# Performance work log

Measured on AMD Instinct MI355X. Metric: run time of the kernel, lower is better.

## Reference

```python
import jax, jax.numpy as jnp
import numpy as np


def setup_inputs() -> dict:
    key = jax.random.key(0)
    k1, k2 = jax.random.split(key)
    B, S_ENC, S_DEC, D = 8, 2048, 2048, 512
    enc_outputs = jax.random.normal(k1, (B, S_ENC, D), dtype=jnp.float32)
    dec_outputs = jax.random.normal(k2, (B, S_DEC, D), dtype=jnp.float32)
    return {"enc_outputs": enc_outputs, "dec_outputs": dec_outputs}


def reference(enc_outputs, dec_outputs):
    # scores: [B, S_dec, S_enc] = dec @ enc^T  (no scaling, no mask — matches original)
    s_t = jnp.einsum('bqd,bkd->bqk', dec_outputs, enc_outputs)
    a_t = jax.nn.softmax(s_t, axis=-1)
    # context: [B, S_dec, D]
    c_t = jnp.einsum('bqk,bkd->bqd', a_t, enc_outputs)
    return c_t
```

## Files before the change

kernel.cpp:

```cpp
#include <hip/hip_runtime.h>
#include <cstdint>
#include <cstddef>

#define Bb 8
#define Ss 2048
#define Dd 512

typedef _Float16 half8 __attribute__((ext_vector_type(8)));
typedef _Float16 half4_ __attribute__((ext_vector_type(4)));
typedef _Float16 half2_t __attribute__((ext_vector_type(2)));
typedef float f32x4 __attribute__((ext_vector_type(4)));

static __device__ __forceinline__ void gload_lds16(const void* g, void* l) {
  __builtin_amdgcn_global_load_lds((const __attribute__((address_space(1))) void*)g,
                                   (__attribute__((address_space(3))) void*)l,
                                   16, 0, 0);
}

__global__ void k0_cvt(const float* __restrict__ in, _Float16* __restrict__ out, int n8) {
  int i = blockIdx.x * blockDim.x + threadIdx.x;
  if (i >= n8) return;
  const float4* p = (const float4*)in + (size_t)i * 2;
  float4 a = p[0], b = p[1];
  half8 h;
  h[0] = (_Float16)a.x; h[1] = (_Float16)a.y; h[2] = (_Float16)a.z; h[3] = (_Float16)a.w;
  h[4] = (_Float16)b.x; h[5] = (_Float16)b.y; h[6] = (_Float16)b.z; h[7] = (_Float16)b.w;
  *(half8*)(out + (size_t)i * 8) = h;
}

__global__ void k0_enc(const float* __restrict__ enc, _Float16* __restrict__ enc16,
                       _Float16* __restrict__ encT) {
  __shared__ float tile[32][33];
  int bid = blockIdx.x;
  int b = bid & 7, kt = (bid >> 3) & 63, dt = bid >> 9;
  int key0 = kt * 32, d0 = dt * 32;
  int t = threadIdx.x;
  const float* src = enc + ((size_t)b * Ss + key0) * Dd + d0;
  _Float16* dst = enc16 + ((size_t)b * Ss + key0) * Dd + d0;
#pragma unroll
  for (int p = 0; p < 4; ++p) {
    int idx = t + p * 256;
    int r = idx >> 5, c = idx & 31;
    float v = src[(size_t)r * Dd + c];
    tile[r][c] = v;
    dst[(size_t)r * Dd + c] = (_Float16)v;
  }
  __syncthreads();
  {
    int dr = t >> 3, kq = t & 7;
    _Float16* o = encT + ((size_t)b * Dd + d0 + dr) * Ss + key0 + kq * 4;
    half4_ v;
#pragma unroll
    for (int j = 0; j < 4; ++j) v[j] = (_Float16)tile[kq * 4 + j][dr];
    *(half4_*)o = v;
  }
}

__launch_bounds__(256, 2)
__global__ void k1_qk(const _Float16* __restrict__ A, const _Float16* __restrict__ Bm,
                      _Float16* __restrict__ S, half2_t* __restrict__ pms) {
  __shared__ __align__(16) _Float16 lA[128 * 64];
  __shared__ __align__(16) _Float16 lB[128 * 64];
  int bid = blockIdx.x;
  int b = bid & 7;
  int t = bid >> 3;
  int tm = t & 15, tn = t >> 4;
  int tid = threadIdx.x;
  int w = tid >> 6, L = tid & 63;
  int wm = w & 1, wn = w >> 1;

  const _Float16* Ag = A + ((size_t)b * Ss + (size_t)tm * 128) * Dd;
  const _Float16* Bg = Bm + ((size_t)b * Ss + (size_t)tn * 128) * Dd;

  int rowS[4], colS[4], ldsOff[4];
#pragma unroll
  for (int i = 0; i < 4; ++i) {
    int se = (w * 4 + i) * 512 + L * 8;
    int row = se >> 6;
    int blk = (se >> 3) & 7;
    rowS[i] = row;
    colS[i] = (blk ^ (row & 7)) << 3;
    ldsOff[i] = se;
  }

  f32x4 acc[4][4];
#pragma unroll
  for (int mt = 0; mt < 4; ++mt)
#pragma unroll
    for (int nt = 0; nt < 4; ++nt) acc[mt][nt] = (f32x4){0.f, 0.f, 0.f, 0.f};

  int g = L >> 4, lm = L & 15;

  for (int k0 = 0; k0 < Dd; k0 += 64) {
    __syncthreads();
#pragma unroll
    for (int i = 0; i < 4; ++i) {
      gload_lds16(Ag + (size_t)rowS[i] * Dd + k0 + colS[i], lA + ldsOff[i]);
      gload_lds16(Bg + (size_t)rowS[i] * Dd + k0 + colS[i], lB + ldsOff[i]);
    }
    __syncthreads();
#pragma unroll
    for (int ds = 0; ds < 64; ds += 32) {
      half8 af[4], bf[4];
#pragma unroll
      for (int mt = 0; mt < 4; ++mt) {
        int row = wm * 64 + mt * 16 + lm;
        int blk = ((ds >> 3) + g) ^ (row & 7);
        af[mt] = *(const half8*)(lA + row * 64 + blk * 8);
      }
#pragma unroll
      for (int nt = 0; nt < 4; ++nt) {
        int row = wn * 64 + nt * 16 + lm;
        int blk = ((ds >> 3) + g) ^ (row & 7);
        bf[nt] = *(const half8*)(lB + row * 64 + blk * 8);
      }
#pragma unroll
      for (int mt = 0; mt < 4; ++mt)
#pragma unroll
        for (int nt = 0; nt < 4; ++nt)
          acc[mt][nt] = __builtin_amdgcn_mfma_f32_16x16x32_f16(af[mt], bf[nt], acc[mt][nt], 0, 0, 0);
    }
  }

  size_t rowbase = (size_t)b * Ss;
#pragma unroll
  for (int mt = 0; mt < 4; ++mt) {
#pragma unroll
    for (int r = 0; r < 4; ++r) {
      int row_g = tm * 128 + wm * 64 + mt * 16 + g * 4 + r;
      _Float16* Srow = S + (rowbase + row_g) * Ss + (size_t)tn * 128 + wn * 64 + lm;
      float rm = -1e30f;
#pragma unroll
      for (int nt = 0; nt < 4; ++nt) rm = fmaxf(rm, acc[mt][nt][r]);
      rm = fmaxf(rm, __shfl_xor(rm, 1));
      rm = fmaxf(rm, __shfl_xor(rm, 2));
      rm = fmaxf(rm, __shfl_xor(rm, 4));
      rm = fmaxf(rm, __shfl_xor(rm, 8));
      _Float16 mh = (_Float16)rm;
      float mf = (float)mh;
      float sum = 0.f;
#pragma unroll
      for (int nt = 0; nt < 4; ++nt) {
        float e = __expf(acc[mt][nt][r] - mf);
        Srow[nt * 16] = (_Float16)e;
        sum += e;
      }
      sum += __shfl_xor(sum, 1);
      sum += __shfl_xor(sum, 2);
      sum += __shfl_xor(sum, 4);
      sum += __shfl_xor(sum, 8);
      if (lm == 0) {
        half2_t st; st.x = mh; st.y = (_Float16)sum;
        pms[(rowbase + row_g) * 32 + tn * 2 + wn] = st;
      }
    }
  }
}

__global__ void k2_factors(const half2_t* __restrict__ pms, float* __restrict__ fct) {
  int t = threadIdx.x;
  size_t row = (size_t)blockIdx.x * 8 + (t >> 5);
  int c = t & 31;
  half2_t v = pms[row * 32 + c];
  float mc = (float)v.x, sc = (float)v.y;
  float m = mc;
#pragma unroll
  for (int d = 1; d <= 16; d <<= 1) m = fmaxf(m, __shfl_xor(m, d));
  float tot = sc * __expf(mc - m);
#pragma unroll
  for (int d = 1; d <= 16; d <<= 1) tot += __shfl_xor(tot, d);
  fct[(size_t)c * (Bb * Ss) + row] = __expf(mc - m) / tot;
}

__launch_bounds__(256, 2)
__global__ void k3_pv(const _Float16* __restrict__ P, const _Float16* __restrict__ Vt,
                      const float* __restrict__ fct, float* __restrict__ C) {
  __shared__ __align__(16) _Float16 lA[128 * 64];
  __shared__ __align__(16) _Float16 lB[128 * 64];
  int bid = blockIdx.x;
  int b = bid & 7;
  int t = bid >> 3;
  int tm = t & 15, tn = t >> 4;
  int tid = threadIdx.x;
  int w = tid >> 6, L = tid & 63;
  int wm = w & 1, wn = w >> 1;

  const _Float16* Ag = P + ((size_t)b * Ss + (size_t)tm * 128) * Ss;
  const _Float16* Bg = Vt + ((size_t)b * Dd + (size_t)tn * 128) * Ss;

  int rowS[4], colS[4], ldsOff[4];
#pragma unroll
  for (int i = 0; i < 4; ++i) {
    int se = (w * 4 + i) * 512 + L * 8;
    int row = se >> 6;
    int blk = (se >> 3) & 7;
    rowS[i] = row;
    colS[i] = (blk ^ (row & 7)) << 3;
    ldsOff[i] = se;
  }

  f32x4 acc[4][4];
#pragma unroll
  for (int mt = 0; mt < 4; ++mt)
#pragma unroll
    for (int nt = 0; nt < 4; ++nt) acc[mt][nt] = (f32x4){0.f, 0.f, 0.f, 0.f};

  int g = L >> 4, lm = L & 15;
  const float* fbase = fct + (size_t)b * Ss + (size_t)tm * 128 + wm * 64 + lm;

  for (int k0 = 0; k0 < Ss; k0 += 64) {
    __syncthreads();
#pragma unroll
    for (int i = 0; i < 4; ++i) {
      gload_lds16(Ag + (size_t)rowS[i] * Ss + k0 + colS[i], lA + ldsOff[i]);
      gload_lds16(Bg + (size_t)rowS[i] * Ss + k0 + colS[i], lB + ldsOff[i]);
    }
    _Float16 fh[4];
#pragma unroll
    for (int mt = 0; mt < 4; ++mt)
      fh[mt] = (_Float16)fbase[(size_t)(k0 >> 6) * (Bb * Ss) + mt * 16];
    __syncthreads();
#pragma unroll
    for (int ds = 0; ds < 64; ds += 32) {
      half8 af[4], bf[4];
#pragma unroll
      for (int mt = 0; mt < 4; ++mt) {
        int row = wm * 64 + mt * 16 + lm;
        int blk = ((ds >> 3) + g) ^ (row & 7);
        af[mt] = *(const half8*)(lA + row * 64 + blk * 8);
#pragma unroll
        for (int j = 0; j < 8; ++j) af[mt][j] *= fh[mt];
      }
#pragma unroll
      for (int nt = 0; nt < 4; ++nt) {
        int row = wn * 64 + nt * 16 + lm;
        int blk = ((ds >> 3) + g) ^ (row & 7);
        bf[nt] = *(const half8*)(lB + row * 64 + blk * 8);
      }
#pragma unroll
      for (int mt = 0; mt < 4; ++mt)
#pragma unroll
        for (int nt = 0; nt < 4; ++nt)
          acc[mt][nt] = __builtin_amdgcn_mfma_f32_16x16x32_f16(af[mt], bf[nt], acc[mt][nt], 0, 0, 0);
    }
  }

#pragma unroll
  for (int mt = 0; mt < 4; ++mt) {
#pragma unroll
    for (int r = 0; r < 4; ++r) {
      int row_g = tm * 128 + wm * 64 + mt * 16 + g * 4 + r;
      float* Crow = C + ((size_t)b * Ss + row_g) * Dd + (size_t)tn * 128 + wn * 64 + lm;
#pragma unroll
      for (int nt = 0; nt < 4; ++nt) Crow[nt * 16] = acc[mt][nt][r];
    }
  }
}

extern "C" void kernel_launch(void* const* d_in, const int* in_sizes, int n_in,
                              void* d_out, int out_size, void* d_ws, size_t ws_size,
                              hipStream_t stream) {
  const float* enc = (const float*)d_in[0];
  const float* dec = (const float*)d_in[1];
  float* out = (float*)d_out;

  const size_t nElem = (size_t)Bb * Ss * Dd;
  const size_t nS = (size_t)Bb * Ss * Ss;

  _Float16* dec16 = (_Float16*)d_ws;
  _Float16* enc16 = dec16 + nElem;
  _Float16* encT = enc16 + nElem;
  _Float16* Sp = encT + nElem;
  half2_t* pms = (half2_t*)(Sp + nS);
  float* fct = (float*)dec16;

  size_t need = nElem * 2 * 3 + nS * 2 + (size_t)Bb * Ss * 32 * 4;
  if (ws_size < need) return;

  k0_cvt<<<(int)(nElem / 8 / 256), 256, 0, stream>>>(dec, dec16, (int)(nElem / 8));
  k0_enc<<<8 * 64 * 16, 256, 0, stream>>>(enc, enc16, encT);
  k1_qk<<<2048, 256, 0, stream>>>(dec16, enc16, Sp, pms);
  k2_factors<<<2048, 256, 0, stream>>>(pms, fct);
  k3_pv<<<512, 256, 0, stream>>>(Sp, encT, fct, out);
}
```

Before: 215.9 us.

## Fuse dec conversion into enc prep and fold softmax factors into PV

```diff
diff --git a/kernel.cpp b/kernel.cpp
--- a/kernel.cpp
+++ b/kernel.cpp
@@ -17,24 +17,23 @@
                                    16, 0, 0);
 }
 
-__global__ void k0_cvt(const float* __restrict__ in, _Float16* __restrict__ out, int n8) {
-  int i = blockIdx.x * blockDim.x + threadIdx.x;
-  if (i >= n8) return;
-  const float4* p = (const float4*)in + (size_t)i * 2;
-  float4 a = p[0], b = p[1];
-  half8 h;
-  h[0] = (_Float16)a.x; h[1] = (_Float16)a.y; h[2] = (_Float16)a.z; h[3] = (_Float16)a.w;
-  h[4] = (_Float16)b.x; h[5] = (_Float16)b.y; h[6] = (_Float16)b.z; h[7] = (_Float16)b.w;
-  *(half8*)(out + (size_t)i * 8) = h;
-}
-
-__global__ void k0_enc(const float* __restrict__ enc, _Float16* __restrict__ enc16,
-                       _Float16* __restrict__ encT) {
+__global__ void k0_prep(const float* __restrict__ enc, const float* __restrict__ dec,
+                        _Float16* __restrict__ enc16, _Float16* __restrict__ encT,
+                        _Float16* __restrict__ dec16) {
   __shared__ float tile[32][33];
   int bid = blockIdx.x;
   int b = bid & 7, kt = (bid >> 3) & 63, dt = bid >> 9;
   int key0 = kt * 32, d0 = dt * 32;
   int t = threadIdx.x;
+
+  {
+    size_t off = (size_t)bid * 1024 + (size_t)t * 4;
+    float4 a = *(const float4*)(dec + off);
+    half4_ h;
+    h[0] = (_Float16)a.x; h[1] = (_Float16)a.y; h[2] = (_Float16)a.z; h[3] = (_Float16)a.w;
+    *(half4_*)(dec16 + off) = h;
+  }
+
   const float* src = enc + ((size_t)b * Ss + key0) * Dd + d0;
   _Float16* dst = enc16 + ((size_t)b * Ss + key0) * Dd + d0;
 #pragma unroll
@@ -157,26 +156,12 @@
   }
 }
 
-__global__ void k2_factors(const half2_t* __restrict__ pms, float* __restrict__ fct) {
-  int t = threadIdx.x;
-  size_t row = (size_t)blockIdx.x * 8 + (t >> 5);
-  int c = t & 31;
-  half2_t v = pms[row * 32 + c];
-  float mc = (float)v.x, sc = (float)v.y;
-  float m = mc;
-#pragma unroll
-  for (int d = 1; d <= 16; d <<= 1) m = fmaxf(m, __shfl_xor(m, d));
-  float tot = sc * __expf(mc - m);
-#pragma unroll
-  for (int d = 1; d <= 16; d <<= 1) tot += __shfl_xor(tot, d);
-  fct[(size_t)c * (Bb * Ss) + row] = __expf(mc - m) / tot;
-}
-
 __launch_bounds__(256, 2)
 __global__ void k3_pv(const _Float16* __restrict__ P, const _Float16* __restrict__ Vt,
-                      const float* __restrict__ fct, float* __restrict__ C) {
+                      const half2_t* __restrict__ pms, float* __restrict__ C) {
   __shared__ __align__(16) _Float16 lA[128 * 64];
   __shared__ __align__(16) _Float16 lB[128 * 64];
+  __shared__ float fctL[32 * 128];
   int bid = blockIdx.x;
   int b = bid & 7;
   int t = bid >> 3;
@@ -185,6 +170,23 @@
   int w = tid >> 6, L = tid & 63;
   int wm = w & 1, wn = w >> 1;
 
+  if (tid < 128) {
+    const half2_t* pr = pms + ((size_t)b * Ss + (size_t)tm * 128 + tid) * 32;
+    float mc[32], sc[32];
+#pragma unroll
+    for (int c = 0; c < 32; ++c) { half2_t v = pr[c]; mc[c] = (float)v.x; sc[c] = (float)v.y; }
+    float m = mc[0];
+#pragma unroll
+    for (int c = 1; c < 32; ++c) m = fmaxf(m, mc[c]);
+    float tot = 0.f;
+    float ef[32];
+#pragma unroll
+    for (int c = 0; c < 32; ++c) { ef[c] = __expf(mc[c] - m); tot += sc[c] * ef[c]; }
+    float rinv = 1.0f / tot;
+#pragma unroll
+    for (int c = 0; c < 32; ++c) fctL[c * 128 + tid] = ef[c] * rinv;
+  }
+
   const _Float16* Ag = P + ((size_t)b * Ss + (size_t)tm * 128) * Ss;
   const _Float16* Bg = Vt + ((size_t)b * Dd + (size_t)tn * 128) * Ss;
 
@@ -206,7 +208,6 @@
     for (int nt = 0; nt < 4; ++nt) acc[mt][nt] = (f32x4){0.f, 0.f, 0.f, 0.f};
 
   int g = L >> 4, lm = L & 15;
-  const float* fbase = fct + (size_t)b * Ss + (size_t)tm * 128 + wm * 64 + lm;
 
   for (int k0 = 0; k0 < Ss; k0 += 64) {
     __syncthreads();
@@ -215,11 +216,11 @@
       gload_lds16(Ag + (size_t)rowS[i] * Ss + k0 + colS[i], lA + ldsOff[i]);
       gload_lds16(Bg + (size_t)rowS[i] * Ss + k0 + colS[i], lB + ldsOff[i]);
     }
+    __syncthreads();
     _Float16 fh[4];
 #pragma unroll
     for (int mt = 0; mt < 4; ++mt)
-      fh[mt] = (_Float16)fbase[(size_t)(k0 >> 6) * (Bb * Ss) + mt * 16];
-    __syncthreads();
+      fh[mt] = (_Float16)fctL[(k0 >> 6) * 128 + wm * 64 + mt * 16 + lm];
 #pragma unroll
     for (int ds = 0; ds < 64; ds += 32) {
       half8 af[4], bf[4];
@@ -272,14 +273,11 @@
   _Float16* encT = enc16 + nElem;
   _Float16* Sp = encT + nElem;
   half2_t* pms = (half2_t*)(Sp + nS);
-  float* fct = (float*)dec16;
 
   size_t need = nElem * 2 * 3 + nS * 2 + (size_t)Bb * Ss * 32 * 4;
   if (ws_size < need) return;
 
-  k0_cvt<<<(int)(nElem / 8 / 256), 256, 0, stream>>>(dec, dec16, (int)(nElem / 8));
-  k0_enc<<<8 * 64 * 16, 256, 0, stream>>>(enc, enc16, encT);
+  k0_prep<<<8192, 256, 0, stream>>>(enc, dec, enc16, encT, dec16);
   k1_qk<<<2048, 256, 0, stream>>>(dec16, enc16, Sp, pms);
-  k2_factors<<<2048, 256, 0, stream>>>(pms, fct);
-  k3_pv<<<512, 256, 0, stream>>>(Sp, encT, fct, out);
-}
+  k3_pv<<<512, 256, 0, stream>>>(Sp, encT, pms, out);
+}
```

Result: faster. 207.5 us (-3.9%).
